# Performance work log

Measured on AMD Instinct MI355X. Metric: run time of the kernel, lower is better.

Reference implementation:

```python
import math
import jax, jax.numpy as jnp
import numpy as np

BATCH, SEQ, D_MODEL, NUM_HEADS = 4, 2048, 1024, 16
D_K = D_MODEL // NUM_HEADS


def setup_inputs() -> dict:
    key = jax.random.key(0)
    ks = jax.random.split(key, 11)
    s = 0.02
    inp = {
        'encodings_q': jax.random.normal(ks[0], (BATCH, SEQ, D_MODEL), jnp.float32),
        'encodings_k': jax.random.normal(ks[1], (BATCH, SEQ, D_MODEL), jnp.float32),
        'encodings_v': jax.random.normal(ks[2], (BATCH, SEQ, D_MODEL), jnp.float32),
        # causal mask: True = masked out (matches masked_fill semantics)
        'mask': jnp.broadcast_to(jnp.triu(jnp.ones((SEQ, SEQ), bool), k=1),
                                 (BATCH, SEQ, SEQ)),
        'Wq': jax.random.normal(ks[3], (D_MODEL, D_MODEL), jnp.float32) * s,
        'bq': jnp.zeros((D_MODEL,), jnp.float32),
        'Wk': jax.random.normal(ks[4], (D_MODEL, D_MODEL), jnp.float32) * s,
        'bk': jnp.zeros((D_MODEL,), jnp.float32),
        'Wv': jax.random.normal(ks[5], (D_MODEL, D_MODEL), jnp.float32) * s,
        'bv': jnp.zeros((D_MODEL,), jnp.float32),
        'Wo': jax.random.normal(ks[6], (D_MODEL, D_MODEL), jnp.float32) * s,
        'bo': jnp.zeros((D_MODEL,), jnp.float32),
    }
    return inp


def reference(encodings_q, encodings_k, encodings_v, mask,
              Wq, bq, Wk, bk, Wv, bv, Wo, bo):
    B, S, D = encodings_q.shape
    H, Dk = NUM_HEADS, D_K
    # projections (nn.Linear: x @ W.T + b), split heads -> (B, H, S, Dk)
    q = (encodings_q @ Wq.T + bq).reshape(B, S, H, Dk).transpose(0, 2, 1, 3)
    k = (encodings_k @ Wk.T + bk).reshape(B, S, H, Dk).transpose(0, 2, 1, 3)
    v = (encodings_v @ Wv.T + bv).reshape(B, S, H, Dk).transpose(0, 2, 1, 3)
    scores = jnp.einsum('bhqd,bhkd->bhqk', q, k) / math.sqrt(Dk)
    # mask dim == 3 -> unsqueeze head dim; masked_fill(mask, -1e9)
    scores = jnp.where(mask[:, None, :, :], jnp.float32(-1e9), scores)
    weights = jax.nn.softmax(scores, axis=-1)
    attn = jnp.einsum('bhqk,bhkd->bhqd', weights, v)
    attn = attn.transpose(0, 2, 1, 3).reshape(B, S, D)
    return attn @ Wo.T + bo
```

## Files before the change

kernel.cpp:

```cpp
#include <hip/hip_runtime.h>
#include <hip/hip_bf16.h>
#include <cstdint>

typedef __bf16 bf16;
typedef bf16  bf16x4 __attribute__((ext_vector_type(4)));
typedef bf16  bf16x8 __attribute__((ext_vector_type(8)));
typedef float f32x4  __attribute__((ext_vector_type(4)));

#define MFMA16(a, b, c) __builtin_amdgcn_mfma_f32_16x16x32_bf16((a), (b), (c), 0, 0, 0)

constexpr int BATCH = 4;
constexpr int SEQ   = 2048;
constexpr int DM    = 1024;
constexpr int NH    = 16;
constexpr int DK    = 64;

__device__ __forceinline__ void gld_lds16(const void* g, void* l) {
    __builtin_amdgcn_global_load_lds(
        (const __attribute__((address_space(1))) unsigned int*)(uintptr_t)g,
        (__attribute__((address_space(3))) unsigned int*)(uintptr_t)l,
        16, 0, 0);
}

__device__ __forceinline__ bf16x8 cvt8(const float* __restrict__ p) {
    f32x4 a = *(const f32x4*)p;
    f32x4 b = *(const f32x4*)(p + 4);
    bf16x8 r;
    r[0] = (bf16)a[0]; r[1] = (bf16)a[1]; r[2] = (bf16)a[2]; r[3] = (bf16)a[3];
    r[4] = (bf16)b[0]; r[5] = (bf16)b[1]; r[6] = (bf16)b[2]; r[7] = (bf16)b[3];
    return r;
}

__global__ __launch_bounds__(256)
void cvt_all(const float* __restrict__ xq, const float* __restrict__ xk,
             const float* __restrict__ xv,
             const float* __restrict__ wq, const float* __restrict__ wk,
             const float* __restrict__ wv, const float* __restrict__ wo,
             bf16* __restrict__ X3, bf16* __restrict__ WB)
{
    const int bid = blockIdx.x;
    const float* s;
    bf16* d;
    int local;
    if (bid < 12288) {
        const int which = bid >> 12;
        local = bid & 4095;
        s = (which == 0) ? xq : (which == 1) ? xk : xv;
        d = X3 + (size_t)which * ((size_t)BATCH * SEQ * DM);
    } else {
        const int b2 = bid - 12288;
        const int which = b2 >> 9;
        local = b2 & 511;
        s = (which == 0) ? wq : (which == 1) ? wk : (which == 2) ? wv : wo;
        d = WB + (size_t)which * (size_t)(DM * DM);
    }
    const size_t i = ((size_t)local * 256 + threadIdx.x) * 8;
    *(bf16x8*)(d + i) = cvt8(s + i);
}

__global__ __launch_bounds__(256)
void cvt_x(const float* __restrict__ src, bf16* __restrict__ dst) {
    const size_t i = ((size_t)blockIdx.x * 256 + threadIdx.x) * 8;
    *(bf16x8*)(dst + i) = cvt8(src + i);
}

__global__ __launch_bounds__(256)
void cvt_w4(const float* __restrict__ s0, const float* __restrict__ s1,
            const float* __restrict__ s2, const float* __restrict__ s3,
            bf16* __restrict__ dst) {
    const float* s = (blockIdx.y == 0) ? s0 : (blockIdx.y == 1) ? s1
                   : (blockIdx.y == 2) ? s2 : s3;
    const size_t i = ((size_t)blockIdx.x * 256 + threadIdx.x) * 8;
    *(bf16x8*)(dst + (size_t)blockIdx.y * (1024 * 1024) + i) = cvt8(s + i);
}

template <int MODE>
__device__ __forceinline__
void gemm_core(const bf16* __restrict__ A, const bf16* __restrict__ W,
               const float* __restrict__ bias, void* __restrict__ outp,
               int m0, int n0, bf16* As, bf16* Bs)
{
    const int tid  = threadIdx.x;
    const int lane = tid & 63;
    const int wave = tid >> 6;
    const int wm   = (wave >> 1) * 64;
    const int wn   = (wave & 1) * 64;
    const int q4   = lane >> 4;
    const int r    = lane & 15;
    const int srow = lane >> 2;
    const int scol = (lane & 3) * 8;

    f32x4 acc[4][4];
#pragma unroll
    for (int i = 0; i < 4; i++)
#pragma unroll
        for (int j = 0; j < 4; j++) acc[i][j] = (f32x4){0.f, 0.f, 0.f, 0.f};

    const bf16* Ag = A + (size_t)(m0 + wave * 32 + srow) * 1024 + scol;
    const bf16* Wg = W + (size_t)(n0 + wave * 32 + srow) * 1024 + scol;
    bf16* AsB = &As[(wave * 32) * 32];
    bf16* BsB = &Bs[(wave * 32) * 32];

    for (int k0 = 0; k0 < 1024; k0 += 32) {
        __syncthreads();
        gld_lds16(Ag + k0,             AsB);
        gld_lds16(Ag + 16 * 1024 + k0, AsB + 16 * 32);
        gld_lds16(Wg + k0,             BsB);
        gld_lds16(Wg + 16 * 1024 + k0, BsB + 16 * 32);
        __syncthreads();

        bf16x8 af[4], bfr[4];
#pragma unroll
        for (int i = 0; i < 4; i++)
            af[i] = *(const bf16x8*)&As[(wm + i * 16 + r) * 32 + q4 * 8];
#pragma unroll
        for (int j = 0; j < 4; j++)
            bfr[j] = *(const bf16x8*)&Bs[(wn + j * 16 + r) * 32 + q4 * 8];
#pragma unroll
        for (int i = 0; i < 4; i++)
#pragma unroll
            for (int j = 0; j < 4; j++) {
                if (MODE == 2)
                    acc[i][j] = MFMA16(af[i], bfr[j], acc[i][j]);
                else
                    acc[i][j] = MFMA16(bfr[j], af[i], acc[i][j]);
            }
    }

    if (MODE == 2) {
#pragma unroll
        for (int j = 0; j < 4; j++) {
            const int col = n0 + wn + j * 16 + r;
            const float bv = bias[col];
            const int hh = col >> 6, d = col & 63;
#pragma unroll
            for (int i = 0; i < 4; i++) {
                const int s0 = m0 + wm + i * 16 + q4 * 4;
                const int b = s0 >> 11, s = s0 & 2047;
                bf16x4 ov;
#pragma unroll
                for (int rr = 0; rr < 4; rr++) ov[rr] = (bf16)(acc[i][j][rr] + bv);
                *(bf16x4*)&((bf16*)outp)[(((size_t)(b * NH + hh)) * DK + d) * SEQ + s] = ov;
            }
        }
    } else {
#pragma unroll
        for (int j = 0; j < 4; j++) {
            const int col0 = n0 + wn + j * 16 + q4 * 4;
            const f32x4 bv4 = *(const f32x4*)&bias[col0];
#pragma unroll
            for (int i = 0; i < 4; i++) {
                const int row = m0 + wm + i * 16 + r;
                if (MODE == 1) {
                    f32x4 ov = acc[i][j] + bv4;
                    *(f32x4*)&((float*)outp)[(size_t)row * 1024 + col0] = ov;
                } else {
                    const int b = row >> 11, s = row & 2047;
                    const int hh = col0 >> 6, d0 = col0 & 63;
                    bf16x4 ov;
#pragma unroll
                    for (int rr = 0; rr < 4; rr++) ov[rr] = (bf16)(acc[i][j][rr] + bv4[rr]);
                    *(bf16x4*)&((bf16*)outp)[(((size_t)(b * NH + hh)) * SEQ + s) * DK + d0] = ov;
                }
            }
        }
    }
}

template <int MODE>
__global__ __launch_bounds__(256)
void gemm_fast(const bf16* __restrict__ A, const bf16* __restrict__ W,
               const float* __restrict__ bias, void* __restrict__ outp)
{
    __shared__ __align__(16) bf16 As[128 * 32];
    __shared__ __align__(16) bf16 Bs[128 * 32];
    gemm_core<MODE>(A, W, bias, outp, blockIdx.x * 128, blockIdx.y * 128, As, Bs);
}

__global__ __launch_bounds__(256)
void gemm_qkv(const bf16* __restrict__ X3, const bf16* __restrict__ WB,
              const float* __restrict__ bq, const float* __restrict__ bk,
              const float* __restrict__ bv,
              bf16* __restrict__ Qt, bf16* __restrict__ Kt, bf16* __restrict__ Vt)
{
    __shared__ __align__(16) bf16 As[128 * 32];
    __shared__ __align__(16) bf16 Bs[128 * 32];
    const int z = blockIdx.z;
    const size_t E = (size_t)BATCH * SEQ * DM, WE = (size_t)DM * DM;
    const bf16* A = X3 + (size_t)z * E;
    const bf16* W = WB + (size_t)z * WE;
    const int m0 = blockIdx.x * 128, n0 = blockIdx.y * 128;
    if (z == 2)
        gemm_core<2>(A, W, bv, Vt, m0, n0, As, Bs);
    else if (z == 1)
        gemm_core<0>(A, W, bk, Kt, m0, n0, As, Bs);
    else
        gemm_core<0>(A, W, bq, Qt, m0, n0, As, Bs);
}

template <int MODE>
__global__ __launch_bounds__(256)
void gemm_slow(const void* __restrict__ Ap, const float* __restrict__ W,
               const float* __restrict__ bias, void* __restrict__ outp)
{
    __shared__ __align__(16) bf16 As[128 * 32];
    __shared__ __align__(16) bf16 Bs[128 * 32];

    const int tid  = threadIdx.x;
    const int lane = tid & 63;
    const int wave = tid >> 6;
    const int wm   = (wave >> 1) * 64;
    const int wn   = (wave & 1) * 64;
    const int m0   = blockIdx.y * 128;
    const int n0   = blockIdx.x * 128;
    const int q    = lane >> 4;
    const int r    = lane & 15;
    const int lrow  = tid >> 2;
    const int lcol8 = (tid & 3) * 8;

    f32x4 acc[4][4];
#pragma unroll
    for (int i = 0; i < 4; i++)
#pragma unroll
        for (int j = 0; j < 4; j++) acc[i][j] = (f32x4){0.f, 0.f, 0.f, 0.f};

    for (int k0 = 0; k0 < 1024; k0 += 32) {
        __syncthreads();
        if (MODE != 1) {
            const float* Af = (const float*)Ap;
            *(bf16x8*)&As[lrow * 32 + lcol8] =
                cvt8(&Af[(size_t)(m0 + lrow) * 1024 + k0 + lcol8]);
            *(bf16x8*)&As[(64 + lrow) * 32 + lcol8] =
                cvt8(&Af[(size_t)(m0 + 64 + lrow) * 1024 + k0 + lcol8]);
        } else {
            const bf16* Ab = (const bf16*)Ap;
            *(bf16x8*)&As[lrow * 32 + lcol8] =
                *(const bf16x8*)&Ab[(size_t)(m0 + lrow) * 1024 + k0 + lcol8];
            *(bf16x8*)&As[(64 + lrow) * 32 + lcol8] =
                *(const bf16x8*)&Ab[(size_t)(m0 + 64 + lrow) * 1024 + k0 + lcol8];
        }
        *(bf16x8*)&Bs[lrow * 32 + lcol8] =
            cvt8(&W[(size_t)(n0 + lrow) * 1024 + k0 + lcol8]);
        *(bf16x8*)&Bs[(64 + lrow) * 32 + lcol8] =
            cvt8(&W[(size_t)(n0 + 64 + lrow) * 1024 + k0 + lcol8]);
        __syncthreads();

        bf16x8 af[4], bfr[4];
#pragma unroll
        for (int i = 0; i < 4; i++)
            af[i] = *(const bf16x8*)&As[(wm + i * 16 + r) * 32 + q * 8];
#pragma unroll
        for (int j = 0; j < 4; j++)
            bfr[j] = *(const bf16x8*)&Bs[(wn + j * 16 + r) * 32 + q * 8];
#pragma unroll
        for (int i = 0; i < 4; i++)
#pragma unroll
            for (int j = 0; j < 4; j++)
                acc[i][j] = MFMA16(af[i], bfr[j], acc[i][j]);
    }

#pragma unroll
    for (int j = 0; j < 4; j++) {
        const int col = n0 + wn + j * 16 + r;
        const float bv = bias[col];
#pragma unroll
        for (int i = 0; i < 4; i++) {
#pragma unroll
            for (int rr = 0; rr < 4; rr++) {
                const int row = m0 + wm + i * 16 + q * 4 + rr;
                const float v = acc[i][j][rr] + bv;
                if (MODE == 1) {
                    ((float*)outp)[(size_t)row * 1024 + col] = v;
                } else {
                    const int b = row >> 11, s = row & 2047;
                    const int hh = col >> 6, d = col & 63;
                    if (MODE == 0)
                        ((bf16*)outp)[(((size_t)(b * NH + hh)) * SEQ + s) * DK + d] = (bf16)v;
                    else
                        ((bf16*)outp)[(((size_t)(b * NH + hh)) * DK + d) * SEQ + s] = (bf16)v;
                }
            }
        }
    }
}

__global__ __launch_bounds__(256)
void attn_causal(const bf16* __restrict__ Qt, const bf16* __restrict__ Kt,
                 const bf16* __restrict__ Vtt, bf16* __restrict__ Ob)
{
    constexpr int LDK = 72;
    __shared__ __align__(16) bf16 Ks[64 * LDK];
    __shared__ __align__(16) bf16 Vs[64 * LDK];
    __shared__ __align__(16) bf16 Ps[4][16 * LDK];

    const int tid  = threadIdx.x;
    const int lane = tid & 63;
    const int wave = tid >> 6;
    const int q4   = lane >> 4;
    const int r    = lane & 15;

    const int bh = blockIdx.x;
    const int qb = blockIdx.y * 64;
    const int b  = bh >> 4;
    const int h  = bh & 15;

    const bf16* Qp = Qt  + ((size_t)bh * SEQ + qb + wave * 16) * DK;
    const bf16* Kp = Kt  + (size_t)bh * SEQ * DK;
    const bf16* Vp = Vtt + (size_t)bh * DK * SEQ;

    bf16x8 qf0 = *(const bf16x8*)&Qp[r * DK + q4 * 8];
    bf16x8 qf1 = *(const bf16x8*)&Qp[r * DK + 32 + q4 * 8];
#pragma unroll
    for (int j = 0; j < 8; j++) {
        qf0[j] = (bf16)((float)qf0[j] * 0.125f);
        qf1[j] = (bf16)((float)qf1[j] * 0.125f);
    }

    bf16x8 ones;
#pragma unroll
    for (int j = 0; j < 8; j++) ones[j] = (bf16)1.0f;

    f32x4 o[4], o5;
#pragma unroll
    for (int i = 0; i < 4; i++) o[i] = (f32x4){0.f, 0.f, 0.f, 0.f};
    o5 = (f32x4){0.f, 0.f, 0.f, 0.f};
    float m_i = -1e30f;

    const int nT   = blockIdx.y + 1;
    const int lrow = tid >> 2;
    const int lcol = (tid & 3) * 16;
    const int qrow = qb + wave * 16 + r;

    for (int t = 0; t < nT; ++t) {
        const int kb = t * 64;
        __syncthreads();
        *(bf16x8*)&Ks[lrow * LDK + lcol] =
            *(const bf16x8*)&Kp[(size_t)(kb + lrow) * DK + lcol];
        *(bf16x8*)&Ks[lrow * LDK + lcol + 8] =
            *(const bf16x8*)&Kp[(size_t)(kb + lrow) * DK + lcol + 8];
        *(bf16x8*)&Vs[lrow * LDK + lcol] =
            *(const bf16x8*)&Vp[(size_t)lrow * SEQ + kb + lcol];
        *(bf16x8*)&Vs[lrow * LDK + lcol + 8] =
            *(const bf16x8*)&Vp[(size_t)lrow * SEQ + kb + lcol + 8];
        __syncthreads();

        f32x4 s[4];
#pragma unroll
        for (int n = 0; n < 4; n++) {
            bf16x8 k0 = *(const bf16x8*)&Ks[(n * 16 + r) * LDK + q4 * 8];
            bf16x8 k1 = *(const bf16x8*)&Ks[(n * 16 + r) * LDK + 32 + q4 * 8];
            f32x4 a = (f32x4){0.f, 0.f, 0.f, 0.f};
            a = MFMA16(k0, qf0, a);
            a = MFMA16(k1, qf1, a);
            s[n] = a;
        }

        float mx = -1e30f;
        if (t == nT - 1) {
#pragma unroll
            for (int n = 0; n < 4; n++) {
                const int c0 = kb + n * 16 + q4 * 4;
#pragma unroll
                for (int rr = 0; rr < 4; rr++) {
                    if (c0 + rr > qrow) s[n][rr] = -1e30f;
                    mx = fmaxf(mx, s[n][rr]);
                }
            }
        } else {
#pragma unroll
            for (int n = 0; n < 4; n++)
#pragma unroll
                for (int rr = 0; rr < 4; rr++)
                    mx = fmaxf(mx, s[n][rr]);
        }
        mx = fmaxf(mx, __shfl_xor(mx, 16, 64));
        mx = fmaxf(mx, __shfl_xor(mx, 32, 64));

        const float mn = fmaxf(m_i, mx);
        const float alpha = __expf(m_i - mn);
        m_i = mn;
#pragma unroll
        for (int n = 0; n < 4; n++)
#pragma unroll
            for (int rr = 0; rr < 4; rr++)
                o[n][rr] *= alpha;
#pragma unroll
        for (int rr = 0; rr < 4; rr++) o5[rr] *= alpha;

        bf16* Pw = &Ps[wave][0];
#pragma unroll
        for (int n = 0; n < 4; n++) {
            bf16x4 pv;
#pragma unroll
            for (int rr = 0; rr < 4; rr++)
                pv[rr] = (bf16)__expf(s[n][rr] - m_i);
            *(bf16x4*)&Pw[r * LDK + n * 16 + q4 * 4] = pv;
        }
        asm volatile("s_waitcnt lgkmcnt(0)" ::: "memory");

#pragma unroll
        for (int kk = 0; kk < 2; kk++) {
            bf16x8 pf = *(const bf16x8*)&Pw[r * LDK + kk * 32 + q4 * 8];
#pragma unroll
            for (int n = 0; n < 4; n++) {
                bf16x8 vf = *(const bf16x8*)&Vs[(n * 16 + r) * LDK + kk * 32 + q4 * 8];
                o[n] = MFMA16(vf, pf, o[n]);
            }
            o5 = MFMA16(ones, pf, o5);
        }
    }

    const float inv = 1.0f / o5[0];
#pragma unroll
    for (int n = 0; n < 4; n++) {
        bf16x4 ov;
#pragma unroll
        for (int rr = 0; rr < 4; rr++) ov[rr] = (bf16)(o[n][rr] * inv);
        *(bf16x4*)&Ob[((size_t)b * SEQ + qrow) * DM + h * DK + n * 16 + q4 * 4] = ov;
    }
}

extern "C" void kernel_launch(void* const* d_in, const int* in_sizes, int n_in,
                              void* d_out, int out_size, void* d_ws, size_t ws_size,
                              hipStream_t stream)
{
    const float* xq = (const float*)d_in[0];
    const float* xk = (const float*)d_in[1];
    const float* xv = (const float*)d_in[2];
    const float* Wq = (const float*)d_in[4];
    const float* bq = (const float*)d_in[5];
    const float* Wk = (const float*)d_in[6];
    const float* bk = (const float*)d_in[7];
    const float* Wv = (const float*)d_in[8];
    const float* bv = (const float*)d_in[9];
    const float* Wo = (const float*)d_in[10];
    const float* bo = (const float*)d_in[11];

    const size_t E  = (size_t)BATCH * SEQ * DM;
    const size_t WE = (size_t)DM * DM;
    bf16* Qt = (bf16*)d_ws;
    bf16* Kt = Qt + E;
    bf16* Vt = Kt + E;
    bf16* Ab = Vt + E;

    dim3 gblk(256);
    dim3 agrid(BATCH * NH, SEQ / 64);

    const size_t need_fused = (7 * E + 4 * WE) * sizeof(bf16);
    const size_t need_fast  = (5 * E + 4 * WE) * sizeof(bf16);

    if (ws_size >= need_fused) {
        bf16* X3 = Ab + E;
        bf16* WB = X3 + 3 * E;

        cvt_all<<<dim3(14336), gblk, 0, stream>>>(xq, xk, xv, Wq, Wk, Wv, Wo, X3, WB);

        gemm_qkv<<<dim3(64, 8, 3), gblk, 0, stream>>>(X3, WB, bq, bk, bv, Qt, Kt, Vt);

        attn_causal<<<agrid, gblk, 0, stream>>>(Qt, Kt, Vt, Ab);

        gemm_fast<1><<<dim3(64, 8), gblk, 0, stream>>>(Ab, WB + 3 * WE, bo, d_out);
    } else if (ws_size >= need_fast) {
        bf16* X  = Ab + E;
        bf16* WB = X + E;

        cvt_w4<<<dim3(512, 4), gblk, 0, stream>>>(Wq, Wk, Wv, Wo, WB);

        cvt_x<<<dim3(4096), gblk, 0, stream>>>(xq, X);
        gemm_fast<0><<<dim3(64, 8), gblk, 0, stream>>>(X, WB + 0 * WE, bq, Qt);
        cvt_x<<<dim3(4096), gblk, 0, stream>>>(xk, X);
        gemm_fast<0><<<dim3(64, 8), gblk, 0, stream>>>(X, WB + 1 * WE, bk, Kt);
        cvt_x<<<dim3(4096), gblk, 0, stream>>>(xv, X);
        gemm_fast<2><<<dim3(64, 8), gblk, 0, stream>>>(X, WB + 2 * WE, bv, Vt);

        attn_causal<<<agrid, gblk, 0, stream>>>(Qt, Kt, Vt, Ab);

        gemm_fast<1><<<dim3(64, 8), gblk, 0, stream>>>(Ab, WB + 3 * WE, bo, d_out);
    } else {
        dim3 ggrid_s(DM / 128, (BATCH * SEQ) / 128);
        gemm_slow<0><<<ggrid_s, gblk, 0, stream>>>(xq, Wq, bq, Qt);
        gemm_slow<0><<<ggrid_s, gblk, 0, stream>>>(xk, Wk, bk, Kt);
        gemm_slow<2><<<ggrid_s, gblk, 0, stream>>>(xv, Wv, bv, Vt);
        attn_causal<<<agrid, gblk, 0, stream>>>(Qt, Kt, Vt, Ab);
        gemm_slow<1><<<ggrid_s, gblk, 0, stream>>>(Ab, Wo, bo, d_out);
    }
}
```

Measured before the change: 373.9 us.

## Load K/V fragments directly from global, reverse tile order, skip redundant rescale

Drops the shared-memory staging of K and V tiles and the two block barriers per iteration. Each wave now reads its MFMA operands straight from global memory and relies on L1/L2 for reuse across the four waves. It also reverses the query-block order so the longest causal blocks launch first, adds an occupancy hint of 6 blocks, and skips the rescale of the accumulators when no row's max increases. The risk is higher global and cache traffic, since each wave re-fetches K/V, and the explicit LDS wait before the P reads is removed.

```diff
diff --git a/kernel.cpp b/kernel.cpp
--- a/kernel.cpp
+++ b/kernel.cpp
@@ -284,13 +284,11 @@
     }
 }
 
-__global__ __launch_bounds__(256)
+__global__ __launch_bounds__(256, 6)
 void attn_causal(const bf16* __restrict__ Qt, const bf16* __restrict__ Kt,
                  const bf16* __restrict__ Vtt, bf16* __restrict__ Ob)
 {
     constexpr int LDK = 72;
-    __shared__ __align__(16) bf16 Ks[64 * LDK];
-    __shared__ __align__(16) bf16 Vs[64 * LDK];
     __shared__ __align__(16) bf16 Ps[4][16 * LDK];
 
     const int tid  = threadIdx.x;
@@ -300,7 +298,8 @@
     const int r    = lane & 15;
 
     const int bh = blockIdx.x;
-    const int qb = blockIdx.y * 64;
+    const int yt = gridDim.y - 1 - blockIdx.y;
+    const int qb = yt * 64;
     const int b  = bh >> 4;
     const int h  = bh & 15;
 
@@ -326,29 +325,18 @@
     o5 = (f32x4){0.f, 0.f, 0.f, 0.f};
     float m_i = -1e30f;
 
-    const int nT   = blockIdx.y + 1;
-    const int lrow = tid >> 2;
-    const int lcol = (tid & 3) * 16;
+    const int nT   = yt + 1;
     const int qrow = qb + wave * 16 + r;
+    bf16* Pw = &Ps[wave][0];
 
     for (int t = 0; t < nT; ++t) {
         const int kb = t * 64;
-        __syncthreads();
-        *(bf16x8*)&Ks[lrow * LDK + lcol] =
-            *(const bf16x8*)&Kp[(size_t)(kb + lrow) * DK + lcol];
-        *(bf16x8*)&Ks[lrow * LDK + lcol + 8] =
-            *(const bf16x8*)&Kp[(size_t)(kb + lrow) * DK + lcol + 8];
-        *(bf16x8*)&Vs[lrow * LDK + lcol] =
-            *(const bf16x8*)&Vp[(size_t)lrow * SEQ + kb + lcol];
-        *(bf16x8*)&Vs[lrow * LDK + lcol + 8] =
-            *(const bf16x8*)&Vp[(size_t)lrow * SEQ + kb + lcol + 8];
-        __syncthreads();
 
         f32x4 s[4];
 #pragma unroll
         for (int n = 0; n < 4; n++) {
-            bf16x8 k0 = *(const bf16x8*)&Ks[(n * 16 + r) * LDK + q4 * 8];
-            bf16x8 k1 = *(const bf16x8*)&Ks[(n * 16 + r) * LDK + 32 + q4 * 8];
+            bf16x8 k0 = *(const bf16x8*)&Kp[(size_t)(kb + n * 16 + r) * DK + q4 * 8];
+            bf16x8 k1 = *(const bf16x8*)&Kp[(size_t)(kb + n * 16 + r) * DK + 32 + q4 * 8];
             f32x4 a = (f32x4){0.f, 0.f, 0.f, 0.f};
             a = MFMA16(k0, qf0, a);
             a = MFMA16(k1, qf1, a);
@@ -376,18 +364,19 @@
         mx = fmaxf(mx, __shfl_xor(mx, 16, 64));
         mx = fmaxf(mx, __shfl_xor(mx, 32, 64));
 
-        const float mn = fmaxf(m_i, mx);
-        const float alpha = __expf(m_i - mn);
-        m_i = mn;
-#pragma unroll
-        for (int n = 0; n < 4; n++)
-#pragma unroll
-            for (int rr = 0; rr < 4; rr++)
-                o[n][rr] *= alpha;
-#pragma unroll
-        for (int rr = 0; rr < 4; rr++) o5[rr] *= alpha;
-
-        bf16* Pw = &Ps[wave][0];
+        if (__ballot(mx > m_i)) {
+            const float mn = fmaxf(m_i, mx);
+            const float alpha = __expf(m_i - mn);
+            m_i = mn;
+#pragma unroll
+            for (int n = 0; n < 4; n++)
+#pragma unroll
+                for (int rr = 0; rr < 4; rr++)
+                    o[n][rr] *= alpha;
+#pragma unroll
+            for (int rr = 0; rr < 4; rr++) o5[rr] *= alpha;
+        }
+
 #pragma unroll
         for (int n = 0; n < 4; n++) {
             bf16x4 pv;
@@ -396,14 +385,13 @@
                 pv[rr] = (bf16)__expf(s[n][rr] - m_i);
             *(bf16x4*)&Pw[r * LDK + n * 16 + q4 * 4] = pv;
         }
-        asm volatile("s_waitcnt lgkmcnt(0)" ::: "memory");
 
 #pragma unroll
         for (int kk = 0; kk < 2; kk++) {
             bf16x8 pf = *(const bf16x8*)&Pw[r * LDK + kk * 32 + q4 * 8];
 #pragma unroll
             for (int n = 0; n < 4; n++) {
-                bf16x8 vf = *(const bf16x8*)&Vs[(n * 16 + r) * LDK + kk * 32 + q4 * 8];
+                bf16x8 vf = *(const bf16x8*)&Vp[(size_t)(n * 16 + r) * SEQ + kb + kk * 32 + q4 * 8];
                 o[n] = MFMA16(vf, pf, o[n]);
             }
             o5 = MFMA16(ones, pf, o5);
```

Measured after the change: 536.3 us. +43.4%, slower.
